# Optimization experiments

Measured on AMD Instinct MI355X. Metric: run time of the kernel, lower is better.

The kernel has to match this reference:

```python
import jax, jax.numpy as jnp
import numpy as np

B, T, D, H, L = 64, 512, 1024, 1024, 2


def _uniform(key, shape, std):
    return jax.random.uniform(key, shape, jnp.float32, -std, std)


def setup_inputs() -> dict:
    key = jax.random.key(0)
    ks = jax.random.split(key, 12)
    std = 1.0 / np.sqrt(H)
    x = jax.random.normal(ks[0], (B, T, D), jnp.float32)
    inp = {"x": x}
    ins = [D, H]
    for i in range(L):
        inp[f"Wx{i}"] = _uniform(ks[1 + 4 * i], (3 * H, ins[i]), std)
        inp[f"bx{i}"] = _uniform(ks[2 + 4 * i], (3 * H,), std)
        inp[f"Wh{i}"] = _uniform(ks[3 + 4 * i], (3 * H, H), std)
        inp[f"bh{i}"] = _uniform(ks[4 + 4 * i], (3 * H,), std)
    inp["fcW"] = _uniform(ks[9], (1, H), 1.0 / np.sqrt(H))
    inp["fcb"] = _uniform(ks[10], (1,), 1.0 / np.sqrt(H))
    return inp


def _gru_cell(x_t, h, Wx, bx, Wh, bh):
    # x_t: [B, in], h: [B, H]
    gx = x_t @ Wx.T + bx  # [B, 3H]
    gh = h @ Wh.T + bh    # [B, 3H]
    i_r, i_z, i_n = jnp.split(gx, 3, axis=1)
    h_r, h_z, h_n = jnp.split(gh, 3, axis=1)
    r = jax.nn.sigmoid(i_r + h_r)
    z = jax.nn.sigmoid(i_z + h_z)
    n = jnp.tanh(i_n + r * h_n)
    return n + z * (h - n)


def reference(x, Wx0, bx0, Wh0, bh0, Wx1, bx1, Wh1, bh1, fcW, fcb):
    params = [(Wx0, bx0, Wh0, bh0), (Wx1, bx1, Wh1, bh1)]
    Bb = x.shape[0]
    h0 = tuple(jnp.zeros((Bb, H), x.dtype) for _ in range(L))

    def step(carry, x_t):
        hs = list(carry)
        inp = x_t
        for i in range(L):
            hs[i] = _gru_cell(inp, hs[i], *params[i])
            inp = hs[i]
        return tuple(hs), None

    xs = jnp.swapaxes(x, 0, 1)  # [T, B, D]
    hs_final, _ = jax.lax.scan(step, h0, xs)
    return hs_final[-1] @ fcW.T + fcb  # [B, 1]
```

## Files before the change

kernel.cpp:

```cpp
#include <hip/hip_runtime.h>

typedef __attribute__((ext_vector_type(8))) short bf8v;
typedef __attribute__((ext_vector_type(4))) float fx4;
typedef unsigned short u16;
typedef unsigned int u32;

constexpr int SP = 1032;

__device__ __forceinline__ float b2f(u16 h) {
    u32 u = ((u32)h) << 16; float f; __builtin_memcpy(&f, &u, 4); return f;
}
__device__ __forceinline__ u16 f2b(float f) {
    u32 u; __builtin_memcpy(&u, &f, 4);
    return (u16)((u + 0x7fffu + ((u >> 16) & 1u)) >> 16);
}

__device__ __forceinline__ float ldsc(const void* p, long off, bool f32) {
    return f32 ? ((const float*)p)[off] : b2f(((const u16*)p)[off]);
}
__device__ __forceinline__ bf8v ld8cv(const void* p, long off, bool f32) {
    if (!f32) return *(const bf8v*)((const u16*)p + off);
    const float* f = (const float*)p + off;
    bf8v r;
#pragma unroll
    for (int j = 0; j < 8; ++j) r[j] = (short)f2b(f[j]);
    return r;
}

__device__ __forceinline__ float gru_out(float sr, float sz, float sn, float xn,
                                         float bxr, float bxz, float bxn,
                                         float bhr, float bhz, float bhn, float hp) {
    float r = 1.f / (1.f + __expf(-(sr + bxr + bhr)));
    float z = 1.f / (1.f + __expf(-(sz + bxz + bhz)));
    float pn = xn + bxn + r * (sn + bhn);
    pn = fminf(fmaxf(pn, -15.f), 15.f);
    float e = __expf(2.f * pn);
    float n = (e - 1.f) / (e + 1.f);
    return n + z * (hp - n);
}

__global__ __launch_bounds__(256) void zero_a(uint4* __restrict__ p) {
    p[(long)blockIdx.x * 256 + threadIdx.x] = make_uint4(0u, 0u, 0u, 0u);
}
__global__ __launch_bounds__(256) void zero_misc(uint4* __restrict__ p) {
    p[(long)blockIdx.x * 256 + threadIdx.x] = make_uint4(0u, 0u, 0u, 0u);
}

__global__ __launch_bounds__(256) void detect_dtype(const u32* __restrict__ x,
                                                    u32* __restrict__ flags) {
    __shared__ int red[256];
    int t = threadIdx.x;
    int cnt = 0;
    for (int i = t; i < 4096; i += 256) {
        u32 ex = (x[i] >> 7) & 0xff;
        cnt += (ex >= 100 && ex <= 135) ? 1 : 0;
    }
    red[t] = cnt; __syncthreads();
    for (int s = 128; s > 0; s >>= 1) { if (t < s) red[t] += red[t + s]; __syncthreads(); }
    if (t == 0) flags[0] = (red[0] < 2048) ? 1u : 0u;
}

__global__ __launch_bounds__(256) void conv_x(const void* __restrict__ x, u16* __restrict__ xc,
                                              const u32* __restrict__ flags) {
    bool f32 = flags[0] != 0;
    long i = ((long)blockIdx.x * 256 + threadIdx.x) * 8;
    if (f32) {
        const float* xf = (const float*)x + i;
        union { u16 o[8]; uint4 v; } u;
#pragma unroll
        for (int j = 0; j < 8; ++j) u.o[j] = f2b(xf[j]);
        *(uint4*)&xc[i] = u.v;
    } else {
        *(uint4*)&xc[i] = *(const uint4*)((const u16*)x + i);
    }
}

__device__ __forceinline__ u32 ldrel(const u32* p) {
    return __hip_atomic_load(p, __ATOMIC_RELAXED, __HIP_MEMORY_SCOPE_AGENT);
}
__device__ __forceinline__ void gbar(u32* bflags, u32* gen, u32 target, int& degraded) {
    const int LIM = degraded ? (1 << 12) : (1 << 20);
    __syncthreads();
    if (threadIdx.x == 0)
        __hip_atomic_store(&bflags[(u32)blockIdx.x * 16u], target,
                           __ATOMIC_RELEASE, __HIP_MEMORY_SCOPE_AGENT);
    if (blockIdx.x == 0) {
        int it = 0;
        while (ldrel(&bflags[(u32)threadIdx.x * 16u]) < target) {
            __builtin_amdgcn_s_sleep(1);
            if (++it > LIM) { degraded = 1; break; }
        }
        (void)__hip_atomic_load(&bflags[(u32)threadIdx.x * 16u],
                                __ATOMIC_ACQUIRE, __HIP_MEMORY_SCOPE_AGENT);
        __syncthreads();
        if (threadIdx.x == 0)
            __hip_atomic_store(gen, target, __ATOMIC_RELEASE, __HIP_MEMORY_SCOPE_AGENT);
    }
    if (threadIdx.x == 0) {
        int it = 0;
        while (ldrel(gen) < target) {
            __builtin_amdgcn_s_sleep(2);
            if (++it > LIM) { degraded = 1; break; }
        }
        (void)__hip_atomic_load(gen, __ATOMIC_ACQUIRE, __HIP_MEMORY_SCOPE_AGENT);
    }
    __syncthreads();
}

template<bool XF32>
__device__ __forceinline__ void gru_step(const short* __restrict__ Wlds,
    const u16* __restrict__ hprev, u16* __restrict__ hout,
    const void* __restrict__ xsrc, long xrow, long hrow,
    int l15, int lk, int bb, int u0,
    float Bxr, float Bxz, float Bxn, float Bhr, float Bhz, float Bhn)
{
    const int koff = lk * 8;

    bf8v bh[8], bx[8];
#pragma unroll
    for (int p = 0; p < 8; ++p) {
        bh[p] = *(const bf8v*)&hprev[hrow + p * 32 + koff];
        if constexpr (XF32) {
            const float* xf = (const float*)xsrc + xrow + p * 32 + koff;
            bf8v tv;
#pragma unroll
            for (int j = 0; j < 8; ++j) tv[j] = (short)f2b(xf[j]);
            bx[p] = tv;
        } else {
            bx[p] = *(const bf8v*)((const u16*)xsrc + xrow + p * 32 + koff);
        }
    }

    fx4 accRZ = {0.f, 0.f, 0.f, 0.f};
    fx4 accNH = {0.f, 0.f, 0.f, 0.f};
    fx4 accNX = {0.f, 0.f, 0.f, 0.f};

#pragma unroll
    for (int i = 0; i < 32; ++i) {
        const int kk = i * 32;
        bf8v rzH = *(const bf8v*)&Wlds[l15 * SP + kk + koff];
        bf8v rzX = *(const bf8v*)&Wlds[(16 + l15) * SP + kk + koff];
        bf8v nW  = *(const bf8v*)&Wlds[(32 + l15) * SP + kk + koff];
        bf8v aH = bh[i & 7], aX = bx[i & 7];
        if (i + 8 < 32) {
            bh[i & 7] = *(const bf8v*)&hprev[hrow + kk + 256 + koff];
            if constexpr (XF32) {
                const float* xf = (const float*)xsrc + xrow + kk + 256 + koff;
                bf8v tv;
#pragma unroll
                for (int j = 0; j < 8; ++j) tv[j] = (short)f2b(xf[j]);
                bx[i & 7] = tv;
            } else {
                bx[i & 7] = *(const bf8v*)((const u16*)xsrc + xrow + kk + 256 + koff);
            }
        }
        accRZ = __builtin_amdgcn_mfma_f32_16x16x32_bf16(aH, rzH, accRZ, 0, 0, 0);
        accRZ = __builtin_amdgcn_mfma_f32_16x16x32_bf16(aX, rzX, accRZ, 0, 0, 0);
        accNH = __builtin_amdgcn_mfma_f32_16x16x32_bf16(aH, nW,  accNH, 0, 0, 0);
        accNX = __builtin_amdgcn_mfma_f32_16x16x32_bf16(aX, nW,  accNX, 0, 0, 0);
    }

#pragma unroll
    for (int reg = 0; reg < 4; ++reg) {
        float sz = __shfl_xor(accRZ[reg], 8);
        float xn = __shfl_xor(accNX[reg], 8);
        if (l15 < 8) {
            const int bi = bb + lk * 4 + reg;
            const long ho = (long)bi * 1024 + u0 + l15;
            float hp = b2f(hprev[ho]);
            float hv = gru_out(accRZ[reg], sz, accNH[reg], xn,
                               Bxr, Bxz, Bxn, Bhr, Bhz, Bhn, hp);
            __builtin_nontemporal_store(f2b(hv), &hout[ho]);
        }
    }
}

__device__ void persist_impl(short* Wlds, bool wf32, bool xf32,
    const void* x, const u16* x16,
    const void* Wx0, const void* Wh0, const void* bx0, const void* bh0,
    const void* Wx1, const void* Wh1, const void* bx1, const void* bh1,
    const u16* zbuf, u16* h0a, u16* h0b, u16* h1a, u16* h1b,
    u32* bflags, u32* gen)
{
    const int blk = blockIdx.x;
    const int layer = blk >> 7;
    const int u0 = (blk & 127) * 8;
    const int tid = threadIdx.x;
    const int l = tid & 63, l15 = l & 15, lk = l >> 4;
    const int w = tid >> 6, bb = w * 16;

    const void* Wh  = layer ? Wh1 : Wh0;
    const void* Wx  = layer ? Wx1 : Wx0;
    const void* bxp = layer ? bx1 : bx0;
    const void* bhp = layer ? bh1 : bh0;

    for (int c = tid; c < 16 * 128; c += 256) {
        int r = c >> 7;
        int kc = (c & 127) * 8;
        int g = r >> 3, j = r & 7;
        long go = (long)(g * 1024 + u0 + j) * 1024 + kc;
        *(bf8v*)&Wlds[r * SP + kc]        = ld8cv(Wh, go, wf32);
        *(bf8v*)&Wlds[(16 + r) * SP + kc] = ld8cv(Wx, go, wf32);
        long gn = (long)(2048 + u0 + j) * 1024 + kc;
        const void* Wn = (r < 8) ? Wh : Wx;
        *(bf8v*)&Wlds[(32 + r) * SP + kc] = ld8cv(Wn, gn, wf32);
    }

    const int uu = u0 + (l15 & 7);
    float Bxr = ldsc(bxp, uu, wf32),        Bhr = ldsc(bhp, uu, wf32);
    float Bxz = ldsc(bxp, 1024 + uu, wf32), Bhz = ldsc(bhp, 1024 + uu, wf32);
    float Bxn = ldsc(bxp, 2048 + uu, wf32), Bhn = ldsc(bhp, 2048 + uu, wf32);
    __syncthreads();

    u16* h0buf[2] = { h0a, h0b };
    u16* h1buf[2] = { h1a, h1b };
    const long hrow = (long)(bb + l15) * 1024;
    int degraded = 0;

    for (int s = 0; s <= 512; ++s) {
        const int t = layer ? (s - 1) : s;
        const bool active = layer ? (s >= 1) : (s < 512);
        if (active) {
            const u16* hprev = (t == 0) ? zbuf
                             : (layer ? h1buf[(t + 1) & 1] : h0buf[(t + 1) & 1]);
            u16* hout = layer ? h1buf[t & 1] : h0buf[t & 1];
            if (layer) {
                gru_step<false>(Wlds, hprev, hout, h0buf[t & 1], hrow, hrow,
                                l15, lk, bb, u0, Bxr, Bxz, Bxn, Bhr, Bhz, Bhn);
            } else {
                const long xrow = ((long)(bb + l15) * 512 + t) * 1024;
                if (xf32)
                    gru_step<true>(Wlds, hprev, hout, x, xrow, hrow,
                                   l15, lk, bb, u0, Bxr, Bxz, Bxn, Bhr, Bhz, Bhn);
                else
                    gru_step<false>(Wlds, hprev, hout, x16, xrow, hrow,
                                    l15, lk, bb, u0, Bxr, Bxz, Bxn, Bhr, Bhz, Bhn);
            }
        }
        gbar(bflags, gen, (u32)(s + 1), degraded);
    }
}

__global__ __launch_bounds__(256, 1) void gru_persist(const void* x, const u16* xc, int xconv,
    const void* Wx0, const void* Wh0, const void* bx0, const void* bh0,
    const void* Wx1, const void* Wh1, const void* bx1, const void* bh1,
    const u16* zbuf, u16* h0a, u16* h0b, u16* h1a, u16* h1b,
    const u32* flags, u32* bflags, u32* gen)
{
    __shared__ __align__(16) short Wlds[48 * SP];
    bool wf32 = flags[0] != 0;
    bool xf32 = wf32 && !xconv;
    const u16* x16 = xconv ? xc : (const u16*)x;
    persist_impl(Wlds, wf32, xf32, x, x16,
                 Wx0, Wh0, bx0, bh0, Wx1, Wh1, bx1, bh1,
                 zbuf, h0a, h0b, h1a, h1b, bflags, gen);
}

__global__ __launch_bounds__(256) void fc_out(const u16* __restrict__ h,
                                              const void* __restrict__ fcW,
                                              const void* __restrict__ fcb,
                                              const u32* __restrict__ flags,
                                              float* __restrict__ out) {
    bool f32 = flags[0] != 0;
    __shared__ float red[256];
    int t = threadIdx.x, b = t >> 2, q = t & 3;
    float s = 0.f;
    for (int u = q * 256; u < q * 256 + 256; ++u) {
        float wv = f32 ? ((const float*)fcW)[u] : b2f(((const u16*)fcW)[u]);
        s += b2f(h[(long)b * 1024 + u]) * wv;
    }
    red[t] = s; __syncthreads();
    if (q == 0) {
        float fb = f32 ? ((const float*)fcb)[0] : b2f(((const u16*)fcb)[0]);
        out[b] = red[t] + red[t + 1] + red[t + 2] + red[t + 3] + fb;
    }
}

extern "C" void kernel_launch(void* const* d_in, const int* in_sizes, int n_in,
                              void* d_out, int out_size, void* d_ws, size_t ws_size,
                              hipStream_t stream) {
    (void)in_sizes; (void)n_in; (void)out_size;
    char* ws = (char*)d_ws;
    u16* zbuf = (u16*)ws;
    u16* h0a  = (u16*)(ws + 131072);
    u16* h0b  = (u16*)(ws + 262144);
    u16* h1a  = (u16*)(ws + 393216);
    u16* h1b  = (u16*)(ws + 524288);
    u32* misc = (u32*)(ws + 655360);
    u32* flags = misc;
    u32* gen   = misc + 16;
    u32* bflags = (u32*)(ws + 659456);
    u16* xc    = (u16*)(ws + 675840);
    const size_t NEED = 675840ull + 67108864ull;
    const int xconv = (ws_size >= NEED) ? 1 : 0;

    zero_a<<<32, 256, 0, stream>>>((uint4*)d_ws);
    zero_misc<<<5, 256, 0, stream>>>((uint4*)(ws + 655360));
    detect_dtype<<<1, 256, 0, stream>>>((const u32*)d_in[0], flags);
    if (xconv) conv_x<<<16384, 256, 0, stream>>>(d_in[0], xc, flags);

    gru_persist<<<256, 256, 0, stream>>>(d_in[0], xc, xconv,
        d_in[1], d_in[3], d_in[2], d_in[4],
        d_in[5], d_in[7], d_in[6], d_in[8],
        zbuf, h0a, h0b, h1a, h1b, flags, bflags, gen);

    fc_out<<<1, 256, 0, stream>>>(h1b, d_in[9], d_in[10], flags, (float*)d_out);
}
```

Before: 9.228 ms.

## Split GRU step K-reduction across two wave groups with LDS reduction

Measured after the change: 10.15 ms. 1.1x slower.

```diff
diff --git a/kernel.cpp b/kernel.cpp
--- a/kernel.cpp
+++ b/kernel.cpp
@@ -85,13 +85,15 @@
         __hip_atomic_store(&bflags[(u32)blockIdx.x * 16u], target,
                            __ATOMIC_RELEASE, __HIP_MEMORY_SCOPE_AGENT);
     if (blockIdx.x == 0) {
-        int it = 0;
-        while (ldrel(&bflags[(u32)threadIdx.x * 16u]) < target) {
-            __builtin_amdgcn_s_sleep(1);
-            if (++it > LIM) { degraded = 1; break; }
-        }
-        (void)__hip_atomic_load(&bflags[(u32)threadIdx.x * 16u],
-                                __ATOMIC_ACQUIRE, __HIP_MEMORY_SCOPE_AGENT);
+        if (threadIdx.x < 256) {
+            int it = 0;
+            while (ldrel(&bflags[(u32)threadIdx.x * 16u]) < target) {
+                __builtin_amdgcn_s_sleep(1);
+                if (++it > LIM) { degraded = 1; break; }
+            }
+            (void)__hip_atomic_load(&bflags[(u32)threadIdx.x * 16u],
+                                    __ATOMIC_ACQUIRE, __HIP_MEMORY_SCOPE_AGENT);
+        }
         __syncthreads();
         if (threadIdx.x == 0)
             __hip_atomic_store(gen, target, __ATOMIC_RELEASE, __HIP_MEMORY_SCOPE_AGENT);
@@ -109,25 +111,33 @@
 
 template<bool XF32>
 __device__ __forceinline__ void gru_step(const short* __restrict__ Wlds,
+    float* __restrict__ Red,
     const u16* __restrict__ hprev, u16* __restrict__ hout,
     const void* __restrict__ xsrc, long xrow, long hrow,
-    int l15, int lk, int bb, int u0,
+    int l15, int lk, int bb, int u0, int kg, int wb, int l,
     float Bxr, float Bxz, float Bxn, float Bhr, float Bhz, float Bhn)
 {
     const int koff = lk * 8;
-
-    bf8v bh[8], bx[8];
-#pragma unroll
-    for (int p = 0; p < 8; ++p) {
-        bh[p] = *(const bf8v*)&hprev[hrow + p * 32 + koff];
+    const int kbase = kg * 512;
+
+    u16 hpr[4];
+#pragma unroll
+    for (int reg = 0; reg < 4; ++reg)
+        hpr[reg] = hprev[(long)(bb + lk * 4 + reg) * 1024 + u0 + (l15 & 7)];
+
+    bf8v bh[16], bx[16];
+#pragma unroll
+    for (int p = 0; p < 16; ++p) {
+        const long ko = kbase + p * 32 + koff;
+        bh[p] = *(const bf8v*)&hprev[hrow + ko];
         if constexpr (XF32) {
-            const float* xf = (const float*)xsrc + xrow + p * 32 + koff;
+            const float* xf = (const float*)xsrc + xrow + ko;
             bf8v tv;
 #pragma unroll
             for (int j = 0; j < 8; ++j) tv[j] = (short)f2b(xf[j]);
             bx[p] = tv;
         } else {
-            bx[p] = *(const bf8v*)((const u16*)xsrc + xrow + p * 32 + koff);
+            bx[p] = *(const bf8v*)((const u16*)xsrc + xrow + ko);
         }
     }
 
@@ -136,46 +146,50 @@
     fx4 accNX = {0.f, 0.f, 0.f, 0.f};
 
 #pragma unroll
-    for (int i = 0; i < 32; ++i) {
-        const int kk = i * 32;
+    for (int c = 0; c < 16; ++c) {
+        const int kk = kbase + c * 32;
         bf8v rzH = *(const bf8v*)&Wlds[l15 * SP + kk + koff];
         bf8v rzX = *(const bf8v*)&Wlds[(16 + l15) * SP + kk + koff];
         bf8v nW  = *(const bf8v*)&Wlds[(32 + l15) * SP + kk + koff];
-        bf8v aH = bh[i & 7], aX = bx[i & 7];
-        if (i + 8 < 32) {
-            bh[i & 7] = *(const bf8v*)&hprev[hrow + kk + 256 + koff];
-            if constexpr (XF32) {
-                const float* xf = (const float*)xsrc + xrow + kk + 256 + koff;
-                bf8v tv;
-#pragma unroll
-                for (int j = 0; j < 8; ++j) tv[j] = (short)f2b(xf[j]);
-                bx[i & 7] = tv;
-            } else {
-                bx[i & 7] = *(const bf8v*)((const u16*)xsrc + xrow + kk + 256 + koff);
+        accRZ = __builtin_amdgcn_mfma_f32_16x16x32_bf16(bh[c], rzH, accRZ, 0, 0, 0);
+        accRZ = __builtin_amdgcn_mfma_f32_16x16x32_bf16(bx[c], rzX, accRZ, 0, 0, 0);
+        accNH = __builtin_amdgcn_mfma_f32_16x16x32_bf16(bh[c], nW,  accNH, 0, 0, 0);
+        accNX = __builtin_amdgcn_mfma_f32_16x16x32_bf16(bx[c], nW,  accNX, 0, 0, 0);
+    }
+
+    float* slot = Red + ((wb * 64 + l) * 12);
+    if (kg == 1) {
+#pragma unroll
+        for (int r = 0; r < 4; ++r) {
+            slot[r]     = accRZ[r];
+            slot[4 + r] = accNH[r];
+            slot[8 + r] = accNX[r];
+        }
+    }
+    __syncthreads();
+    if (kg == 0) {
+#pragma unroll
+        for (int r = 0; r < 4; ++r) {
+            accRZ[r] += slot[r];
+            accNH[r] += slot[4 + r];
+            accNX[r] += slot[8 + r];
+        }
+#pragma unroll
+        for (int reg = 0; reg < 4; ++reg) {
+            float sz = __shfl_xor(accRZ[reg], 8);
+            float xn = __shfl_xor(accNX[reg], 8);
+            if (l15 < 8) {
+                const int bi = bb + lk * 4 + reg;
+                const long ho = (long)bi * 1024 + u0 + l15;
+                float hv = gru_out(accRZ[reg], sz, accNH[reg], xn,
+                                   Bxr, Bxz, Bxn, Bhr, Bhz, Bhn, b2f(hpr[reg]));
+                __builtin_nontemporal_store(f2b(hv), &hout[ho]);
             }
         }
-        accRZ = __builtin_amdgcn_mfma_f32_16x16x32_bf16(aH, rzH, accRZ, 0, 0, 0);
-        accRZ = __builtin_amdgcn_mfma_f32_16x16x32_bf16(aX, rzX, accRZ, 0, 0, 0);
-        accNH = __builtin_amdgcn_mfma_f32_16x16x32_bf16(aH, nW,  accNH, 0, 0, 0);
-        accNX = __builtin_amdgcn_mfma_f32_16x16x32_bf16(aX, nW,  accNX, 0, 0, 0);
-    }
-
-#pragma unroll
-    for (int reg = 0; reg < 4; ++reg) {
-        float sz = __shfl_xor(accRZ[reg], 8);
-        float xn = __shfl_xor(accNX[reg], 8);
-        if (l15 < 8) {
-            const int bi = bb + lk * 4 + reg;
-            const long ho = (long)bi * 1024 + u0 + l15;
-            float hp = b2f(hprev[ho]);
-            float hv = gru_out(accRZ[reg], sz, accNH[reg], xn,
-                               Bxr, Bxz, Bxn, Bhr, Bhz, Bhn, hp);
-            __builtin_nontemporal_store(f2b(hv), &hout[ho]);
-        }
-    }
-}
-
-__device__ void persist_impl(short* Wlds, bool wf32, bool xf32,
+    }
+}
+
+__device__ void persist_impl(short* Wlds, float* Red, bool wf32, bool xf32,
     const void* x, const u16* x16,
     const void* Wx0, const void* Wh0, const void* bx0, const void* bh0,
     const void* Wx1, const void* Wh1, const void* bx1, const void* bh1,
@@ -187,14 +201,14 @@
     const int u0 = (blk & 127) * 8;
     const int tid = threadIdx.x;
     const int l = tid & 63, l15 = l & 15, lk = l >> 4;
-    const int w = tid >> 6, bb = w * 16;
+    const int w6 = tid >> 6, wb = w6 & 3, kg = w6 >> 2, bb = wb * 16;
 
     const void* Wh  = layer ? Wh1 : Wh0;
     const void* Wx  = layer ? Wx1 : Wx0;
     const void* bxp = layer ? bx1 : bx0;
     const void* bhp = layer ? bh1 : bh0;
 
-    for (int c = tid; c < 16 * 128; c += 256) {
+    for (int c = tid; c < 16 * 128; c += 512) {
         int r = c >> 7;
         int kc = (c & 127) * 8;
         int g = r >> 3, j = r & 7;
@@ -225,33 +239,34 @@
                              : (layer ? h1buf[(t + 1) & 1] : h0buf[(t + 1) & 1]);
             u16* hout = layer ? h1buf[t & 1] : h0buf[t & 1];
             if (layer) {
-                gru_step<false>(Wlds, hprev, hout, h0buf[t & 1], hrow, hrow,
-                                l15, lk, bb, u0, Bxr, Bxz, Bxn, Bhr, Bhz, Bhn);
+                gru_step<false>(Wlds, Red, hprev, hout, h0buf[t & 1], hrow, hrow,
+                                l15, lk, bb, u0, kg, wb, l, Bxr, Bxz, Bxn, Bhr, Bhz, Bhn);
             } else {
                 const long xrow = ((long)(bb + l15) * 512 + t) * 1024;
                 if (xf32)
-                    gru_step<true>(Wlds, hprev, hout, x, xrow, hrow,
-                                   l15, lk, bb, u0, Bxr, Bxz, Bxn, Bhr, Bhz, Bhn);
+                    gru_step<true>(Wlds, Red, hprev, hout, x, xrow, hrow,
+                                   l15, lk, bb, u0, kg, wb, l, Bxr, Bxz, Bxn, Bhr, Bhz, Bhn);
                 else
-                    gru_step<false>(Wlds, hprev, hout, x16, xrow, hrow,
-                                    l15, lk, bb, u0, Bxr, Bxz, Bxn, Bhr, Bhz, Bhn);
+                    gru_step<false>(Wlds, Red, hprev, hout, x16, xrow, hrow,
+                                    l15, lk, bb, u0, kg, wb, l, Bxr, Bxz, Bxn, Bhr, Bhz, Bhn);
             }
         }
         gbar(bflags, gen, (u32)(s + 1), degraded);
     }
 }
 
-__global__ __launch_bounds__(256, 1) void gru_persist(const void* x, const u16* xc, int xconv,
+__global__ __launch_bounds__(512, 2) void gru_persist(const void* x, const u16* xc, int xconv,
     const void* Wx0, const void* Wh0, const void* bx0, const void* bh0,
     const void* Wx1, const void* Wh1, const void* bx1, const void* bh1,
     const u16* zbuf, u16* h0a, u16* h0b, u16* h1a, u16* h1b,
     const u32* flags, u32* bflags, u32* gen)
 {
     __shared__ __align__(16) short Wlds[48 * SP];
+    __shared__ __align__(16) float Red[4 * 64 * 12];
     bool wf32 = flags[0] != 0;
     bool xf32 = wf32 && !xconv;
     const u16* x16 = xconv ? xc : (const u16*)x;
-    persist_impl(Wlds, wf32, xf32, x, x16,
+    persist_impl(Wlds, Red, wf32, xf32, x, x16,
                  Wx0, Wh0, bx0, bh0, Wx1, Wh1, bx1, bh1,
                  zbuf, h0a, h0b, h1a, h1b, bflags, gen);
 }
@@ -299,7 +314,7 @@
     detect_dtype<<<1, 256, 0, stream>>>((const u32*)d_in[0], flags);
     if (xconv) conv_x<<<16384, 256, 0, stream>>>(d_in[0], xc, flags);
 
-    gru_persist<<<256, 256, 0, stream>>>(d_in[0], xc, xconv,
+    gru_persist<<<256, 512, 0, stream>>>(d_in[0], xc, xconv,
         d_in[1], d_in[3], d_in[2], d_in[4],
         d_in[5], d_in[7], d_in[6], d_in[8],
         zbuf, h0a, h0b, h1a, h1b, flags, bflags, gen);
```
